# Kernel optimization log

Measured on AMD Instinct MI355X. Metric: run time of the kernel, lower is better.

The kernel has to match this reference:

```python
import math
import jax, jax.numpy as jnp
import numpy as np

MODEL_DIM = 2048
NUM_EXPERTS = 64
NUM_TOKENS = 8192
CAPACITY_FACTOR = 1.0


def setup_inputs() -> dict:
    key = jax.random.key(0)
    kx, kw = jax.random.split(key)
    x = jax.random.normal(kx, (NUM_TOKENS, MODEL_DIM), dtype=jnp.float32)
    # Linear(model_dim, num_experts, bias=False): weight [E, D], y = x @ W.T
    wg = jax.random.normal(kw, (NUM_EXPERTS, MODEL_DIM), dtype=jnp.float32) * (1.0 / math.sqrt(MODEL_DIM))
    return {"x": x, "wg": wg}


def reference(x, wg):
    # ---- gate projection: logits [S, E] ----
    logits = jnp.einsum('sd,ed->se', x, wg)
    gates = jax.nn.softmax(logits, axis=1)
    S, E = gates.shape
    # training mode -> capacity = capacity_factor * ceil(S / E)  (static)
    capacity = int(CAPACITY_FACTOR * math.ceil(S / E))

    # ---- top-1 expert selection ----
    indices1_s = jnp.argmax(gates, axis=1)                      # [S]
    mask1 = jax.nn.one_hot(indices1_s, E, dtype=jnp.int32)      # [S, E]

    # gate value of the chosen expert per token
    gates1_s = jnp.sum(gates * mask1.astype(gates.dtype), axis=1)  # [S]

    # position of each token within its expert's queue (cumsum over tokens)
    locations1 = jnp.cumsum(mask1, axis=0) - 1                  # [S, E]

    # ---- load-balancing auxiliary loss ----
    me = jnp.mean(gates, axis=0)                                # [E]
    ce = jnp.mean(mask1.astype(gates.dtype), axis=0)            # [E]
    l_aux = jnp.mean(me * ce) * (E * E)

    # ---- capacity enforcement: drop tokens beyond expert capacity ----
    mask1 = mask1 * (locations1 < capacity).astype(mask1.dtype) # [S, E]
    locations1_s = jnp.sum(locations1 * mask1, axis=1)          # [S]

    # ---- combine / dispatch tensors ----
    gates1 = gates1_s[:, None] * mask1.astype(gates.dtype)      # [S, E]
    locations1_sc = jax.nn.one_hot(locations1_s, capacity, dtype=gates.dtype)  # [S, C]
    # torch.bmm(gates1[:, :, None], locations1_sc[:, None, :]) == outer product per token
    combine1_sec = jnp.einsum('se,sc->sec', gates1, locations1_sc)  # [S, E, C]
    dispatch_mask = combine1_sec > 0                            # bool [S, E, C]

    return l_aux, combine1_sec, dispatch_mask
```

## Files before the change

kernel.cpp:

```cpp
#include <hip/hip_runtime.h>
#include <math.h>

#define DIM     2048
#define NEXP    64
#define CAP     128
#define NTOK    8192
#define NTILE   256
#define BKC     128
#define WROW    132

#define OUT_LAST   134217728ull
#define NF4        33554432ull

typedef float vfloat4 __attribute__((ext_vector_type(4)));

__global__ __launch_bounds__(256) void fill_out(float* __restrict__ out)
{
    vfloat4* o4 = reinterpret_cast<vfloat4*>(out);
    const vfloat4 z4 = {0.f, 0.f, 0.f, 0.f};
    size_t base = (size_t)blockIdx.x * 16384 + threadIdx.x;
    #pragma unroll 16
    for (int q = 0; q < 64; ++q)
        __builtin_nontemporal_store(z4, &o4[base + ((size_t)q << 8)]);
    if (blockIdx.x == 0 && threadIdx.x == 0)
        out[OUT_LAST] = 0.0f;
}

__global__ __launch_bounds__(512) void gate_kernel(
    const float* __restrict__ x, const float* __restrict__ wg,
    int* __restrict__ expert_idx, float* __restrict__ gate_top,
    float* __restrict__ me_partial, int* __restrict__ counts)
{
    __shared__ __align__(16) float wsmem[NEXP * WROW];
    __shared__ float me_w[8 * NEXP];
    __shared__ int   cnt_w[8 * NEXP];

    const int tid  = threadIdx.x;
    const int gb   = blockIdx.x;
    const int lane = tid & 63;
    const int wv   = __builtin_amdgcn_readfirstlane(tid >> 6);
    const int tok0 = gb * 32 + wv * 4;

    float acc[4] = {};

    for (int kc = 0; kc < DIM / BKC; ++kc) {
        const int k0 = kc * BKC;
        #pragma unroll
        for (int q = 0; q < 4; ++q) {
            int id = tid + (q << 9);
            int e  = id >> 5;
            int c  = id & 31;
            float4 v = *(const float4*)(wg + (size_t)e * DIM + k0 + (c << 2));
            *(float4*)(&wsmem[e * WROW + (c << 2)]) = v;
        }
        __syncthreads();

        #pragma unroll 8
        for (int kk = 0; kk < BKC; kk += 4) {
            float4 w4 = *(const float4*)(&wsmem[lane * WROW + kk]);
            #pragma unroll
            for (int t = 0; t < 4; ++t) {
                float4 xv = *(const float4*)(x + (size_t)(tok0 + t) * DIM + k0 + kk);
                acc[t] = fmaf(xv.x, w4.x, acc[t]);
                acc[t] = fmaf(xv.y, w4.y, acc[t]);
                acc[t] = fmaf(xv.z, w4.z, acc[t]);
                acc[t] = fmaf(xv.w, w4.w, acc[t]);
            }
        }
        __syncthreads();
    }

    float me_acc  = 0.0f;
    int   cnt_acc = 0;
    #pragma unroll
    for (int t = 0; t < 4; ++t) {
        float v = acc[t];
        float m = v; int mi = lane;
        #pragma unroll
        for (int off = 32; off > 0; off >>= 1) {
            float om  = __shfl_xor(m, off);
            int   omi = __shfl_xor(mi, off);
            if (om > m || (om == m && omi < mi)) { m = om; mi = omi; }
        }
        float ex = __expf(v - m);
        float s  = ex;
        #pragma unroll
        for (int off = 32; off > 0; off >>= 1) s += __shfl_xor(s, off);
        me_acc += ex / s;
        if (lane == mi) {
            expert_idx[tok0 + t] = mi;
            gate_top[tok0 + t]   = 1.0f / s;
            ++cnt_acc;
        }
    }
    me_w[wv * NEXP + lane]  = me_acc;
    cnt_w[wv * NEXP + lane] = cnt_acc;
    __syncthreads();
    if (tid < NEXP) {
        float ms = 0.f; int cs = 0;
        #pragma unroll
        for (int w = 0; w < 8; ++w) { ms += me_w[w * NEXP + tid]; cs += cnt_w[w * NEXP + tid]; }
        me_partial[gb * NEXP + tid] = ms;
        counts[gb * NEXP + tid]     = cs;
    }
}

__global__ __launch_bounds__(1024) void prefix_laux(
    const float* __restrict__ me_partial, const int* __restrict__ counts,
    int* __restrict__ block_off, float* __restrict__ out)
{
    __shared__ int   cnt_l[16 * NEXP];
    __shared__ float me_l[16 * NEXP];
    __shared__ int   cnt_tot[NEXP];
    __shared__ float me_tot[NEXP];

    const int tid = threadIdx.x;
    const int e   = tid & 63;
    const int g   = tid >> 6;

    int   cs = 0; float ms = 0.f;
    #pragma unroll
    for (int i = 0; i < 16; ++i) {
        int t = g * 16 + i;
        cs += counts[t * NEXP + e];
        ms += me_partial[t * NEXP + e];
    }
    cnt_l[g * NEXP + e] = cs;
    me_l[g * NEXP + e]  = ms;
    __syncthreads();

    if (g == 0) {
        int run = 0; float mt = 0.f;
        #pragma unroll
        for (int i = 0; i < 16; ++i) {
            int c = cnt_l[i * NEXP + e];
            cnt_l[i * NEXP + e] = run;
            run += c;
            mt  += me_l[i * NEXP + e];
        }
        cnt_tot[e] = run;
        me_tot[e]  = mt;
    }
    __syncthreads();

    int run = cnt_l[g * NEXP + e];
    #pragma unroll
    for (int i = 0; i < 16; ++i) {
        int t = g * 16 + i;
        block_off[t * NEXP + e] = run;
        run += counts[t * NEXP + e];
    }

    if (tid < NEXP) {
        float v = (me_tot[e] / (float)NTOK) * ((float)cnt_tot[e] / (float)NTOK);
        #pragma unroll
        for (int off = 32; off > 0; off >>= 1) v += __shfl_xor(v, off);
        if (e == 0) out[0] = v * (float)NEXP;
    }
}

__global__ __launch_bounds__(64) void scatter_k(
    const int* __restrict__ expert_idx, const float* __restrict__ gate_top,
    const int* __restrict__ block_off, float* __restrict__ out)
{
    __shared__ int es[32];
    int t = threadIdx.x, b = blockIdx.x;
    if (t < 32) es[t] = expert_idx[b * 32 + t];
    __syncthreads();
    if (t < 32) {
        int e = es[t];
        int rank = 0;
        for (int u = 0; u < t; ++u) rank += (es[u] == e) ? 1 : 0;
        int loc = block_off[b * NEXP + e] + rank;
        if (loc < CAP) {
            size_t sidx = (size_t)(b * 32 + t);
            size_t off  = sidx * (NEXP * CAP) + (size_t)e * CAP + loc;
            out[1 + off] = gate_top[b * 32 + t];
            out[1 + (size_t)NTOK * NEXP * CAP + off] = 1.0f;
        }
    }
}

extern "C" void kernel_launch(void* const* d_in, const int* in_sizes, int n_in,
                              void* d_out, int out_size, void* d_ws, size_t ws_size,
                              hipStream_t stream)
{
    const float* x  = (const float*)d_in[0];
    const float* wg = (const float*)d_in[1];
    float* out = (float*)d_out;

    char* ws = (char*)d_ws;
    int*   expert_idx = (int*)  (ws);
    float* gate_top   = (float*)(ws + 32768);
    float* me_partial = (float*)(ws + 65536);
    int*   counts     = (int*)  (ws + 131072);
    int*   block_off  = (int*)  (ws + 196608);

    fill_out<<<2048, 256, 0, stream>>>(out);
    gate_kernel<<<NTILE, 512, 0, stream>>>(x, wg, expert_idx, gate_top,
                                           me_partial, counts);
    prefix_laux<<<1, 1024, 0, stream>>>(me_partial, counts, block_off, out);
    scatter_k<<<NTILE, 64, 0, stream>>>(expert_idx, gate_top, block_off, out);
}
```

Baseline: 728.5 us.

## Register-tile gate GEMM with shared-memory x/w tiles and split-K reduction

Rewrites the gate projection kernel to stage both x and wg chunks in shared memory. Each thread computes an 8x8 register tile of token-by-expert partial dot products over its own slice of K. The eight K-slices are reduced through shared memory before the per-row softmax and argmax. Previously each lane reread x rows from global memory with only 4 accumulators. The aim is more FMA reuse per load, at the cost of high register pressure and fewer threads per block.

```diff
diff --git a/kernel.cpp b/kernel.cpp
--- a/kernel.cpp
+++ b/kernel.cpp
@@ -6,11 +6,12 @@
 #define CAP     128
 #define NTOK    8192
 #define NTILE   256
-#define BKC     128
-#define WROW    132
+#define KC      256
+#define NCH     (DIM/KC)
+#define XWSTR   260
+#define PSTR    68
 
 #define OUT_LAST   134217728ull
-#define NF4        33554432ull
 
 typedef float vfloat4 __attribute__((ext_vector_type(4)));
 
@@ -26,55 +27,102 @@
         out[OUT_LAST] = 0.0f;
 }
 
-__global__ __launch_bounds__(512) void gate_kernel(
+__global__ __launch_bounds__(256, 1) void gate_kernel(
     const float* __restrict__ x, const float* __restrict__ wg,
     int* __restrict__ expert_idx, float* __restrict__ gate_top,
     float* __restrict__ me_partial, int* __restrict__ counts)
 {
-    __shared__ __align__(16) float wsmem[NEXP * WROW];
-    __shared__ float me_w[8 * NEXP];
-    __shared__ int   cnt_w[8 * NEXP];
+    __shared__ __align__(16) float smem[(32 + NEXP) * XWSTR];
+    __shared__ float me_w[4 * NEXP];
+    __shared__ int   cnt_w[4 * NEXP];
+
+    float* xs = smem;
+    float* ws = smem + 32 * XWSTR;
 
     const int tid  = threadIdx.x;
     const int gb   = blockIdx.x;
+    const int tok0 = gb * 32;
+    const int s    = tid >> 5;
+    const int i    = tid & 31;
+    const int tg   = i & 3;
+    const int eg   = i >> 2;
+    const int kb   = s * 32;
+
+    float acc[8][8] = {};
+
+    for (int ch = 0; ch < NCH; ++ch) {
+        const int k0 = ch * KC;
+        #pragma unroll
+        for (int q = 0; q < 8; ++q) {
+            int id = tid + (q << 8);
+            int r = id >> 6, c = id & 63;
+            float4 v = *(const float4*)(x + (size_t)(tok0 + r) * DIM + k0 + 4 * c);
+            *(float4*)(&xs[r * XWSTR + 4 * c]) = v;
+        }
+        #pragma unroll
+        for (int q = 0; q < 16; ++q) {
+            int id = tid + (q << 8);
+            int r = id >> 6, c = id & 63;
+            float4 v = *(const float4*)(wg + (size_t)r * DIM + k0 + 4 * c);
+            *(float4*)(&ws[r * XWSTR + 4 * c]) = v;
+        }
+        __syncthreads();
+
+        for (int q2 = 0; q2 < 8; ++q2) {
+            const int kk = kb + 4 * q2;
+            float4 xt[8], we[8];
+            #pragma unroll
+            for (int j = 0; j < 8; ++j)
+                xt[j] = *(const float4*)(&xs[(tg + 4 * j) * XWSTR + kk]);
+            #pragma unroll
+            for (int m = 0; m < 8; ++m)
+                we[m] = *(const float4*)(&ws[(eg + 8 * m) * XWSTR + kk]);
+            #pragma unroll
+            for (int j = 0; j < 8; ++j)
+                #pragma unroll
+                for (int m = 0; m < 8; ++m) {
+                    acc[j][m] = fmaf(xt[j].x, we[m].x, acc[j][m]);
+                    acc[j][m] = fmaf(xt[j].y, we[m].y, acc[j][m]);
+                    acc[j][m] = fmaf(xt[j].z, we[m].z, acc[j][m]);
+                    acc[j][m] = fmaf(xt[j].w, we[m].w, acc[j][m]);
+                }
+        }
+        __syncthreads();
+    }
+
+    float* part = smem;
+    float* lgt  = smem + 8 * 32 * PSTR;
+    #pragma unroll
+    for (int j = 0; j < 8; ++j)
+        #pragma unroll
+        for (int m = 0; m < 8; ++m)
+            part[(s * 32 + tg + 4 * j) * PSTR + eg + 8 * m] = acc[j][m];
+    __syncthreads();
+
+    {
+        int t  = tid >> 3;
+        int e0 = (tid & 7) * 8;
+        float4 a0 = {0,0,0,0}, a1 = {0,0,0,0};
+        #pragma unroll
+        for (int s2 = 0; s2 < 8; ++s2) {
+            float4 p0 = *(const float4*)(&part[(s2 * 32 + t) * PSTR + e0]);
+            float4 p1 = *(const float4*)(&part[(s2 * 32 + t) * PSTR + e0 + 4]);
+            a0.x += p0.x; a0.y += p0.y; a0.z += p0.z; a0.w += p0.w;
+            a1.x += p1.x; a1.y += p1.y; a1.z += p1.z; a1.w += p1.w;
+        }
+        __syncthreads();
+        *(float4*)(&lgt[t * PSTR + e0])     = a0;
+        *(float4*)(&lgt[t * PSTR + e0 + 4]) = a1;
+    }
+    __syncthreads();
+
     const int lane = tid & 63;
-    const int wv   = __builtin_amdgcn_readfirstlane(tid >> 6);
-    const int tok0 = gb * 32 + wv * 4;
-
-    float acc[4] = {};
-
-    for (int kc = 0; kc < DIM / BKC; ++kc) {
-        const int k0 = kc * BKC;
-        #pragma unroll
-        for (int q = 0; q < 4; ++q) {
-            int id = tid + (q << 9);
-            int e  = id >> 5;
-            int c  = id & 31;
-            float4 v = *(const float4*)(wg + (size_t)e * DIM + k0 + (c << 2));
-            *(float4*)(&wsmem[e * WROW + (c << 2)]) = v;
-        }
-        __syncthreads();
-
-        #pragma unroll 8
-        for (int kk = 0; kk < BKC; kk += 4) {
-            float4 w4 = *(const float4*)(&wsmem[lane * WROW + kk]);
-            #pragma unroll
-            for (int t = 0; t < 4; ++t) {
-                float4 xv = *(const float4*)(x + (size_t)(tok0 + t) * DIM + k0 + kk);
-                acc[t] = fmaf(xv.x, w4.x, acc[t]);
-                acc[t] = fmaf(xv.y, w4.y, acc[t]);
-                acc[t] = fmaf(xv.z, w4.z, acc[t]);
-                acc[t] = fmaf(xv.w, w4.w, acc[t]);
-            }
-        }
-        __syncthreads();
-    }
-
+    const int wv   = tid >> 6;
     float me_acc  = 0.0f;
     int   cnt_acc = 0;
-    #pragma unroll
-    for (int t = 0; t < 4; ++t) {
-        float v = acc[t];
+    for (int r8 = 0; r8 < 8; ++r8) {
+        int row = wv * 8 + r8;
+        float v = lgt[row * PSTR + lane];
         float m = v; int mi = lane;
         #pragma unroll
         for (int off = 32; off > 0; off >>= 1) {
@@ -83,13 +131,13 @@
             if (om > m || (om == m && omi < mi)) { m = om; mi = omi; }
         }
         float ex = __expf(v - m);
-        float s  = ex;
-        #pragma unroll
-        for (int off = 32; off > 0; off >>= 1) s += __shfl_xor(s, off);
-        me_acc += ex / s;
+        float sm = ex;
+        #pragma unroll
+        for (int off = 32; off > 0; off >>= 1) sm += __shfl_xor(sm, off);
+        me_acc += ex / sm;
         if (lane == mi) {
-            expert_idx[tok0 + t] = mi;
-            gate_top[tok0 + t]   = 1.0f / s;
+            expert_idx[tok0 + row] = mi;
+            gate_top[tok0 + row]   = 1.0f / sm;
             ++cnt_acc;
         }
     }
@@ -97,11 +145,10 @@
     cnt_w[wv * NEXP + lane] = cnt_acc;
     __syncthreads();
     if (tid < NEXP) {
-        float ms = 0.f; int cs = 0;
-        #pragma unroll
-        for (int w = 0; w < 8; ++w) { ms += me_w[w * NEXP + tid]; cs += cnt_w[w * NEXP + tid]; }
-        me_partial[gb * NEXP + tid] = ms;
-        counts[gb * NEXP + tid]     = cs;
+        me_partial[gb * NEXP + tid] = me_w[tid] + me_w[NEXP + tid]
+                                    + me_w[2 * NEXP + tid] + me_w[3 * NEXP + tid];
+        counts[gb * NEXP + tid]     = cnt_w[tid] + cnt_w[NEXP + tid]
+                                    + cnt_w[2 * NEXP + tid] + cnt_w[3 * NEXP + tid];
     }
 }
 
@@ -118,7 +165,7 @@
     const int e   = tid & 63;
     const int g   = tid >> 6;
 
-    int   cs = 0; float ms = 0.f;
+    int cs = 0; float ms = 0.f;
     #pragma unroll
     for (int i = 0; i < 16; ++i) {
         int t = g * 16 + i;
@@ -197,7 +244,7 @@
     int*   block_off  = (int*)  (ws + 196608);
 
     fill_out<<<2048, 256, 0, stream>>>(out);
-    gate_kernel<<<NTILE, 512, 0, stream>>>(x, wg, expert_idx, gate_top,
+    gate_kernel<<<NTILE, 256, 0, stream>>>(x, wg, expert_idx, gate_top,
                                            me_partial, counts);
     prefix_laux<<<1, 1024, 0, stream>>>(me_partial, counts, block_off, out);
     scatter_k<<<NTILE, 64, 0, stream>>>(expert_idx, gate_top, block_off, out);
```

Result: faster. 615.5 us (-15.5%).
